# Kernel tuning notes

Hardware: AMD Instinct MI355X
Metric: run time of the kernel (lower is better)

## Reference

```python
import jax, jax.numpy as jnp
import numpy as np

NUM_HEADS = 8
KEY_DIM = 16
D_HEAD = 64  # attn_ratio(4) * key_dim


def setup_inputs() -> dict:
    key = jax.random.key(0)
    ks = jax.random.split(key, 13)
    f = jnp.float32
    x = jax.random.normal(ks[0], (2, 256, 56, 56), dtype=f)
    wq = jax.random.normal(ks[1], (128, 256), dtype=f) * 0.05
    sq = jax.random.uniform(ks[2], (128,), dtype=f)
    bq = jax.random.normal(ks[3], (128,), dtype=f) * 0.05
    wk = jax.random.normal(ks[4], (128, 256), dtype=f) * 0.05
    sk = jax.random.uniform(ks[5], (128,), dtype=f)
    bk = jax.random.normal(ks[6], (128,), dtype=f) * 0.05
    wv = jax.random.normal(ks[7], (512, 256), dtype=f) * 0.05
    sv = jax.random.uniform(ks[8], (512,), dtype=f)
    bv = jax.random.normal(ks[9], (512,), dtype=f) * 0.05
    wp = jax.random.normal(ks[10], (256, 512), dtype=f) * 0.05
    sp = jax.random.uniform(ks[11], (256,), dtype=f)
    bp = jax.random.normal(ks[12], (256,), dtype=f) * 0.05
    return dict(x=x, wq=wq, sq=sq, bq=bq, wk=wk, sk=sk, bk=bk,
                wv=wv, sv=sv, bv=bv, wp=wp, sp=sp, bp=bp)


def _conv1x1_bn(x, w, s, b):
    # 1x1 conv (no bias) + folded BatchNorm (eval): per-channel affine
    y = jnp.einsum('oc,bchw->bohw', w, x)
    return y * s[None, :, None, None] + b[None, :, None, None]


def reference(x, wq, sq, bq, wk, sk, bk, wv, sv, bv, wp, sp, bp):
    b, c, h, w = x.shape
    n = h * w
    q = _conv1x1_bn(x, wq, sq, bq).reshape(b, NUM_HEADS, KEY_DIM, n)
    k = _conv1x1_bn(x, wk, sk, bk).reshape(b, NUM_HEADS, KEY_DIM, n)
    v = _conv1x1_bn(x, wv, sv, bv).reshape(b, NUM_HEADS, D_HEAD, n)
    # scores: q^T k, NO 1/sqrt(key_dim) scaling (faithful to source)
    attn = jax.nn.softmax(jnp.einsum('bhdn,bhdm->bhnm', q, k), axis=-1)
    # out = attn @ v^T -> (b,h,n,d), then back to (b, dh, H, W)
    o = jnp.einsum('bhnm,bhdm->bhdn', attn, v).reshape(b, NUM_HEADS * D_HEAD, h, w)
    return _conv1x1_bn(o, wp, sp, bp)
```

## Files before the change

### kernel.cpp

```cpp
#include <hip/hip_runtime.h>


typedef short  s16x8 __attribute__((ext_vector_type(8)));
typedef float  f32x4 __attribute__((ext_vector_type(4)));
typedef unsigned short u16;
typedef unsigned short u16x4 __attribute__((ext_vector_type(4)));

__device__ __forceinline__ u16 f2bf(float f) {
    unsigned u = __builtin_bit_cast(unsigned, f);
    u += 0x7FFF + ((u >> 16) & 1);
    return (u16)(u >> 16);
}
__device__ __forceinline__ u16 f2bf_h(float f) {
    unsigned u = __builtin_bit_cast(unsigned, f);
    return (u16)((u + 0x8000) >> 16);
}
__device__ __forceinline__ f32x4 mfma32(s16x8 a, s16x8 b, f32x4 c) {
    return __builtin_amdgcn_mfma_f32_16x16x32_bf16(a, b, c, 0, 0, 0);
}

__global__ __launch_bounds__(256) void xtw_kernel(
    const float* __restrict__ x, u16* __restrict__ xpk,
    const float* __restrict__ wq, const float* __restrict__ sq,
    const float* __restrict__ wk, const float* __restrict__ sk,
    const float* __restrict__ wv, const float* __restrict__ sv,
    const float* __restrict__ wp, const float* __restrict__ sp,
    u16* __restrict__ wqpk, u16* __restrict__ wkpk,
    u16* __restrict__ wvpk, u16* __restrict__ wppk)
{
    const int t = threadIdx.x;
    if (blockIdx.z == 2) {
        int ch = (blockIdx.y * 49 + blockIdx.x) * 256 + t;
        const float *W, *S; u16* dst; int nkc;
        if (ch < 4096)        { W = wq; S = sq; dst = wqpk; nkc = 8; }
        else if (ch < 8192)   { W = wk; S = sk; dst = wkpk; nkc = 8;  ch -= 4096; }
        else if (ch < 24576)  { W = wv; S = sv; dst = wvpk; nkc = 8;  ch -= 8192; }
        else if (ch < 40960)  { W = wp; S = sp; dst = wppk; nkc = 16; ch -= 24576; }
        else return;
        const int lane = ch & 63, kc = (ch >> 6) % nkc, rt = (ch >> 6) / nkc;
        const int l15 = lane & 15, q = lane >> 4;
        const int row = rt * 16 + l15, C = nkc * 32;
        const float sc = S[row];
        const float* src = &W[row * C + kc * 32 + q * 8];
        s16x8 o;
        #pragma unroll
        for (int j = 0; j < 8; j++) o[j] = (short)f2bf(src[j] * sc);
        *(s16x8*)&dst[ch * 8] = o;
        return;
    }
    const int b = blockIdx.z, c0 = blockIdx.y * 64, n0 = blockIdx.x * 64;
    __shared__ float lds[64][65];
    const int nl = t & 63, cl = t >> 6;
    #pragma unroll
    for (int i = 0; i < 16; i++) {
        const int c = cl + i * 4;
        lds[c][nl] = x[(b * 256 + c0 + c) * 3136 + n0 + nl];
    }
    __syncthreads();
    #pragma unroll
    for (int rep = 0; rep < 2; rep++) {
        const int idx = rep * 256 + t;
        const int t16l = idx >> 7, kc8l = (idx >> 6) & 1, lane = idx & 63;
        const int l15 = lane & 15, q = lane >> 4;
        s16x8 o;
        #pragma unroll
        for (int j = 0; j < 8; j++)
            o[j] = (short)f2bf(lds[kc8l * 32 + q * 8 + j][t16l * 16 + l15]);
        const int tg = (n0 >> 4) + t16l, kg = (c0 >> 5) + kc8l;
        *(s16x8*)&xpk[(((b * 196 + tg) * 8 + kg) * 64 + lane) * 8] = o;
    }
}

__global__ __launch_bounds__(256, 4) void qkv_kernel(
    const u16* __restrict__ xpk,
    const u16* __restrict__ wqpk, const u16* __restrict__ wkpk, const u16* __restrict__ wvpk,
    const float* __restrict__ bq, const float* __restrict__ bk, const float* __restrict__ bv,
    u16* __restrict__ qws, u16* __restrict__ kws, u16* __restrict__ vpk)
{
    const int b = blockIdx.z, rt = blockIdx.y, n0 = blockIdx.x * 64;
    const int t = threadIdx.x, wave = t >> 6, lane = t & 63;
    const int l15 = lane & 15, quad = lane >> 4;
    const f32x4 z = {0.f, 0.f, 0.f, 0.f};

    if (rt < 4) {
        const u16* wb      = (rt < 2) ? wqpk : wkpk;
        const float* bias  = (rt < 2) ? bq : bk;
        u16* dst           = (rt < 2) ? qws : kws;
        const float qs     = (rt < 2) ? 1.44269504088896f : 1.0f;
        const int och0 = (rt & 1) * 64;
        const int m0   = n0 + wave * 16;
        const int m_t  = blockIdx.x * 4 + wave;
        s16x8 a8[8];
        #pragma unroll
        for (int kc8 = 0; kc8 < 8; kc8++)
            a8[kc8] = *(const s16x8*)&xpk[(((b * 196 + m_t) * 8 + kc8) * 64 + lane) * 8];
        f32x4 acc[4] = {z, z, z, z};
        #pragma unroll
        for (int kc8 = 0; kc8 < 8; kc8++) {
            #pragma unroll
            for (int f = 0; f < 4; f++) {
                s16x8 bf = *(const s16x8*)&wb[((((rt & 1) * 4 + f) * 8 + kc8) * 64 + lane) * 8];
                acc[f] = mfma32(a8[kc8], bf, acc[f]);
            }
        }
        #pragma unroll
        for (int f = 0; f < 4; f++) {
            const int och = och0 + f * 16 + l15;
            const float bi = bias[och];
            const int h = och >> 4;
            #pragma unroll
            for (int r = 0; r < 4; r++) {
                const int tok = m0 + quad * 4 + r;
                dst[((b * 8 + h) * 3136 + tok) * 16 + l15] = f2bf((acc[f][r] + bi) * qs);
            }
        }
    } else {
        const int h    = rt - 4;
        const int och0 = h * 64 + wave * 16;
        s16x8 a8[8];
        #pragma unroll
        for (int kc8 = 0; kc8 < 8; kc8++)
            a8[kc8] = *(const s16x8*)&wvpk[(((h * 4 + wave) * 8 + kc8) * 64 + lane) * 8];
        f32x4 acc[4] = {z, z, z, z};
        #pragma unroll
        for (int kc8 = 0; kc8 < 8; kc8++) {
            #pragma unroll
            for (int f = 0; f < 4; f++) {
                s16x8 bf = *(const s16x8*)&xpk[(((b * 196 + blockIdx.x * 4 + f) * 8 + kc8) * 64 + lane) * 8];
                acc[f] = mfma32(a8[kc8], bf, acc[f]);
            }
        }
        u16* vdst = &vpk[(((b * 8 + h) * 49 + blockIdx.x) * 8) * 512];
        #pragma unroll
        for (int r = 0; r < 4; r++) {
            const float bi = bv[och0 + quad * 4 + r];
            const int lane_r8 = ((l15 >> 2) * 16 + quad * 4 + r) * 8;
            #pragma unroll
            for (int f = 0; f < 4; f++) {
                const int idx = ((f >> 1) * 4 + wave) * 512 + lane_r8 + (f & 1) * 4 + (l15 & 3);
                vdst[idx] = f2bf(acc[f][r] + bi);
            }
        }
    }
}

__global__ __launch_bounds__(64) void attn_kernel(
    const u16* __restrict__ qws, const u16* __restrict__ kws,
    const u16* __restrict__ vpk, u16* __restrict__ opk)
{
    const int bh   = blockIdx.x;
    const int nb   = blockIdx.y * 32;
    const int lane = threadIdx.x;
    const int l15  = lane & 15, quad = lane >> 4;

    s16x8 aq[2];
    #pragma unroll
    for (int u = 0; u < 2; u++) {
        aq[u] = (s16x8){0, 0, 0, 0, 0, 0, 0, 0};
        if (quad < 2)
            aq[u] = *(const s16x8*)&qws[(bh * 3136 + nb + u * 16 + l15) * 16 + quad * 8];
    }
    s16x8 ones;
    #pragma unroll
    for (int i = 0; i < 8; i++) ones[i] = (short)0x3F80;

    const u16* krow = &kws[(bh * 3136 + l15) * 16 + (quad & 1) * 8];
    const u16* vb   = &vpk[bh * 49 * 4096 + lane * 8];

    f32x4 acc[2][4], acc5[2];
    #pragma unroll
    for (int u = 0; u < 2; u++) {
        #pragma unroll
        for (int dt = 0; dt < 4; dt++) acc[u][dt] = (f32x4){0.f, 0.f, 0.f, 0.f};
        acc5[u] = (f32x4){0.f, 0.f, 0.f, 0.f};
    }
    const f32x4 z = {0.f, 0.f, 0.f, 0.f};

    s16x8 kfA[4], vfA[8], kfB[4], vfB[8];
    auto loadK = [&](s16x8* kf, int c) {
        #pragma unroll
        for (int ii = 0; ii < 4; ii++)
            kf[ii] = *(const s16x8*)&krow[(c * 64 + ii * 16) * 16];
    };
    auto loadV = [&](s16x8* vf, int c) {
        #pragma unroll
        for (int i = 0; i < 8; i++)
            vf[i] = *(const s16x8*)&vb[(c * 8 + i) * 512];
    };
    auto compute = [&](const s16x8* kf, const s16x8* vf) {
        #pragma unroll
        for (int u = 0; u < 2; u++) {
            f32x4 s[4];
            #pragma unroll
            for (int ii = 0; ii < 4; ii++) s[ii] = mfma32(kf[ii], aq[u], z);
            s16x8 pf[2];
            #pragma unroll
            for (int c32 = 0; c32 < 2; c32++) {
                #pragma unroll
                for (int r = 0; r < 4; r++) {
                    pf[c32][r]     = (short)f2bf_h(__builtin_amdgcn_exp2f(s[2 * c32][r]));
                    pf[c32][4 + r] = (short)f2bf_h(__builtin_amdgcn_exp2f(s[2 * c32 + 1][r]));
                }
            }
            #pragma unroll
            for (int c32 = 0; c32 < 2; c32++) {
                #pragma unroll
                for (int dt = 0; dt < 4; dt++)
                    acc[u][dt] = mfma32(vf[c32 * 4 + dt], pf[c32], acc[u][dt]);
                acc5[u] = mfma32(ones, pf[c32], acc5[u]);
            }
        }
    };

    loadK(kfA, 0); loadV(vfA, 0);
    #pragma unroll 1
    for (int c = 0; c < 49; c += 2) {
        if (c + 1 < 49) { loadK(kfB, c + 1); loadV(vfB, c + 1); }
        compute(kfA, vfA);
        if (c + 2 < 49) { loadK(kfA, c + 2); loadV(vfA, c + 2); }
        if (c + 1 < 49) compute(kfB, vfB);
    }

    const int bq_ = bh >> 3, h = bh & 7;
    #pragma unroll
    for (int u = 0; u < 2; u++) {
        const float inv = 1.0f / acc5[u][0];
        const int tt = blockIdx.y * 2 + u;
        u16* ob = &opk[((bq_ * 196 + tt) * 16) * 512];
        #pragma unroll
        for (int dt = 0; dt < 4; dt++) {
            u16x4 o4;
            #pragma unroll
            for (int r = 0; r < 4; r++) o4[r] = f2bf(acc[u][dt][r] * inv);
            *(u16x4*)&ob[(h * 2 + (dt >> 1)) * 512 +
                         (((dt & 1) * 2 + (quad >> 1)) * 16 + l15) * 8 +
                         (quad & 1) * 4] = o4;
        }
    }
}

__global__ __launch_bounds__(256, 4) void proj_kernel(
    const u16* __restrict__ opk, const u16* __restrict__ wppk,
    const float* __restrict__ bp, float* __restrict__ out)
{
    const int b = blockIdx.z, n0 = blockIdx.x * 32;
    const int och0 = blockIdx.y * 64 + (threadIdx.x >> 6) * 16;
    const int lane = threadIdx.x & 63;
    const int l15 = lane & 15, quad = lane >> 4;
    const f32x4 z = {0.f, 0.f, 0.f, 0.f};

    const int och_t = blockIdx.y * 4 + (threadIdx.x >> 6);
    s16x8 a8[16];
    #pragma unroll
    for (int kc = 0; kc < 16; kc++)
        a8[kc] = *(const s16x8*)&wppk[((och_t * 16 + kc) * 64 + lane) * 8];
    f32x4 acc[2] = {z, z};
    #pragma unroll
    for (int kc = 0; kc < 16; kc++) {
        #pragma unroll
        for (int f = 0; f < 2; f++) {
            s16x8 bf = *(const s16x8*)&opk[(((b * 196 + blockIdx.x * 2 + f) * 16 + kc) * 64 + lane) * 8];
            acc[f] = mfma32(a8[kc], bf, acc[f]);
        }
    }
    #pragma unroll
    for (int r = 0; r < 4; r++) {
        const int och = och0 + quad * 4 + r;
        const float bi = bp[och];
        #pragma unroll
        for (int f = 0; f < 2; f++)
            out[(b * 256 + och) * 3136 + n0 + f * 16 + l15] = acc[f][r] + bi;
    }
}

extern "C" void kernel_launch(void* const* d_in, const int* in_sizes, int n_in,
                              void* d_out, int out_size, void* d_ws, size_t ws_size,
                              hipStream_t stream) {
    const float* x  = (const float*)d_in[0];
    const float* wq = (const float*)d_in[1];
    const float* sq = (const float*)d_in[2];
    const float* bq = (const float*)d_in[3];
    const float* wk = (const float*)d_in[4];
    const float* sk = (const float*)d_in[5];
    const float* bk = (const float*)d_in[6];
    const float* wv = (const float*)d_in[7];
    const float* sv = (const float*)d_in[8];
    const float* bv = (const float*)d_in[9];
    const float* wp = (const float*)d_in[10];
    const float* sp = (const float*)d_in[11];
    const float* bp = (const float*)d_in[12];
    float* out = (float*)d_out;

    u16* qws  = (u16*)d_ws;
    u16* kws  = qws + 802816;
    u16* vpk  = kws + 802816;
    u16* R    = vpk + 3211264;
    u16* xpk  = R;
    u16* opk  = R;
    u16* wqpk = R + 3211264;
    u16* wkpk = wqpk + 32768;
    u16* wvpk = wkpk + 32768;
    u16* wppk = wvpk + 131072;

    xtw_kernel<<<dim3(49, 4, 3), 256, 0, stream>>>(x, xpk, wq, sq, wk, sk,
                                                   wv, sv, wp, sp,
                                                   wqpk, wkpk, wvpk, wppk);
    qkv_kernel<<<dim3(49, 12, 2), 256, 0, stream>>>(xpk, wqpk, wkpk, wvpk,
                                                    bq, bk, bv, qws, kws, vpk);
    attn_kernel<<<dim3(16, 98), 64, 0, stream>>>(qws, kws, vpk, opk);
    proj_kernel<<<dim3(98, 4, 2), 256, 0, stream>>>(opk, wppk, bp, out);
}
```

Measured before the change: 152.2 us.

## Halve attention query tile per wave, use packed bf16 convert and setprio around MFMAs

The attention kernel now handles 16 query rows per 64-thread block instead of 32, doubling the grid to 16x196 blocks to raise occupancy and parallelism. In exchange, K and V tiles are reloaded twice as often for the same queries. The manual bf16 rounding of exp results is replaced by the packed v_cvt_pk_bf16_f32 instruction, cutting VALU work. s_setprio is raised around the PV MFMA block to favor matrix issue among co-resident waves.

```diff
diff --git a/kernel.cpp b/kernel.cpp
--- a/kernel.cpp
+++ b/kernel.cpp
@@ -3,6 +3,7 @@
 
 typedef short  s16x8 __attribute__((ext_vector_type(8)));
 typedef float  f32x4 __attribute__((ext_vector_type(4)));
+typedef int    i32x4 __attribute__((ext_vector_type(4)));
 typedef unsigned short u16;
 typedef unsigned short u16x4 __attribute__((ext_vector_type(4)));
 
@@ -11,12 +12,13 @@
     u += 0x7FFF + ((u >> 16) & 1);
     return (u16)(u >> 16);
 }
-__device__ __forceinline__ u16 f2bf_h(float f) {
-    unsigned u = __builtin_bit_cast(unsigned, f);
-    return (u16)((u + 0x8000) >> 16);
-}
 __device__ __forceinline__ f32x4 mfma32(s16x8 a, s16x8 b, f32x4 c) {
     return __builtin_amdgcn_mfma_f32_16x16x32_bf16(a, b, c, 0, 0, 0);
+}
+__device__ __forceinline__ int cvtpk(float lo, float hi) {
+    int r;
+    asm("v_cvt_pk_bf16_f32 %0, %1, %2" : "=v"(r) : "v"(lo), "v"(hi));
+    return r;
 }
 
 __global__ __launch_bounds__(256) void xtw_kernel(
@@ -149,17 +151,13 @@
     const u16* __restrict__ vpk, u16* __restrict__ opk)
 {
     const int bh   = blockIdx.x;
-    const int nb   = blockIdx.y * 32;
+    const int nb   = blockIdx.y * 16;
     const int lane = threadIdx.x;
     const int l15  = lane & 15, quad = lane >> 4;
 
-    s16x8 aq[2];
-    #pragma unroll
-    for (int u = 0; u < 2; u++) {
-        aq[u] = (s16x8){0, 0, 0, 0, 0, 0, 0, 0};
-        if (quad < 2)
-            aq[u] = *(const s16x8*)&qws[(bh * 3136 + nb + u * 16 + l15) * 16 + quad * 8];
-    }
+    s16x8 aq = {0, 0, 0, 0, 0, 0, 0, 0};
+    if (quad < 2)
+        aq = *(const s16x8*)&qws[(bh * 3136 + nb + l15) * 16 + quad * 8];
     s16x8 ones;
     #pragma unroll
     for (int i = 0; i < 8; i++) ones[i] = (short)0x3F80;
@@ -167,13 +165,10 @@
     const u16* krow = &kws[(bh * 3136 + l15) * 16 + (quad & 1) * 8];
     const u16* vb   = &vpk[bh * 49 * 4096 + lane * 8];
 
-    f32x4 acc[2][4], acc5[2];
-    #pragma unroll
-    for (int u = 0; u < 2; u++) {
-        #pragma unroll
-        for (int dt = 0; dt < 4; dt++) acc[u][dt] = (f32x4){0.f, 0.f, 0.f, 0.f};
-        acc5[u] = (f32x4){0.f, 0.f, 0.f, 0.f};
-    }
+    f32x4 acc[4], acc5;
+    #pragma unroll
+    for (int dt = 0; dt < 4; dt++) acc[dt] = (f32x4){0.f, 0.f, 0.f, 0.f};
+    acc5 = (f32x4){0.f, 0.f, 0.f, 0.f};
     const f32x4 z = {0.f, 0.f, 0.f, 0.f};
 
     s16x8 kfA[4], vfA[8], kfB[4], vfB[8];
@@ -188,28 +183,34 @@
             vf[i] = *(const s16x8*)&vb[(c * 8 + i) * 512];
     };
     auto compute = [&](const s16x8* kf, const s16x8* vf) {
-        #pragma unroll
-        for (int u = 0; u < 2; u++) {
-            f32x4 s[4];
-            #pragma unroll
-            for (int ii = 0; ii < 4; ii++) s[ii] = mfma32(kf[ii], aq[u], z);
-            s16x8 pf[2];
-            #pragma unroll
-            for (int c32 = 0; c32 < 2; c32++) {
-                #pragma unroll
-                for (int r = 0; r < 4; r++) {
-                    pf[c32][r]     = (short)f2bf_h(__builtin_amdgcn_exp2f(s[2 * c32][r]));
-                    pf[c32][4 + r] = (short)f2bf_h(__builtin_amdgcn_exp2f(s[2 * c32 + 1][r]));
-                }
-            }
-            #pragma unroll
-            for (int c32 = 0; c32 < 2; c32++) {
-                #pragma unroll
-                for (int dt = 0; dt < 4; dt++)
-                    acc[u][dt] = mfma32(vf[c32 * 4 + dt], pf[c32], acc[u][dt]);
-                acc5[u] = mfma32(ones, pf[c32], acc5[u]);
-            }
-        }
+        f32x4 s[4];
+        #pragma unroll
+        for (int ii = 0; ii < 4; ii++) s[ii] = mfma32(kf[ii], aq, z);
+        float e[4][4];
+        #pragma unroll
+        for (int ii = 0; ii < 4; ii++)
+            #pragma unroll
+            for (int r = 0; r < 4; r++)
+                e[ii][r] = __builtin_amdgcn_exp2f(s[ii][r]);
+        s16x8 pf[2];
+        #pragma unroll
+        for (int c32 = 0; c32 < 2; c32++) {
+            i32x4 pk;
+            pk[0] = cvtpk(e[2 * c32][0],     e[2 * c32][1]);
+            pk[1] = cvtpk(e[2 * c32][2],     e[2 * c32][3]);
+            pk[2] = cvtpk(e[2 * c32 + 1][0], e[2 * c32 + 1][1]);
+            pk[3] = cvtpk(e[2 * c32 + 1][2], e[2 * c32 + 1][3]);
+            pf[c32] = __builtin_bit_cast(s16x8, pk);
+        }
+        __builtin_amdgcn_s_setprio(1);
+        #pragma unroll
+        for (int c32 = 0; c32 < 2; c32++) {
+            #pragma unroll
+            for (int dt = 0; dt < 4; dt++)
+                acc[dt] = mfma32(vf[c32 * 4 + dt], pf[c32], acc[dt]);
+            acc5 = mfma32(ones, pf[c32], acc5);
+        }
+        __builtin_amdgcn_s_setprio(0);
     };
 
     loadK(kfA, 0); loadV(vfA, 0);
@@ -222,20 +223,16 @@
     }
 
     const int bq_ = bh >> 3, h = bh & 7;
-    #pragma unroll
-    for (int u = 0; u < 2; u++) {
-        const float inv = 1.0f / acc5[u][0];
-        const int tt = blockIdx.y * 2 + u;
-        u16* ob = &opk[((bq_ * 196 + tt) * 16) * 512];
-        #pragma unroll
-        for (int dt = 0; dt < 4; dt++) {
-            u16x4 o4;
-            #pragma unroll
-            for (int r = 0; r < 4; r++) o4[r] = f2bf(acc[u][dt][r] * inv);
-            *(u16x4*)&ob[(h * 2 + (dt >> 1)) * 512 +
-                         (((dt & 1) * 2 + (quad >> 1)) * 16 + l15) * 8 +
-                         (quad & 1) * 4] = o4;
-        }
+    const float inv = 1.0f / acc5[0];
+    u16* ob = &opk[((bq_ * 196 + blockIdx.y) * 16) * 512];
+    #pragma unroll
+    for (int dt = 0; dt < 4; dt++) {
+        u16x4 o4;
+        #pragma unroll
+        for (int r = 0; r < 4; r++) o4[r] = f2bf(acc[dt][r] * inv);
+        *(u16x4*)&ob[(h * 2 + (dt >> 1)) * 512 +
+                     (((dt & 1) * 2 + (quad >> 1)) * 16 + l15) * 8 +
+                     (quad & 1) * 4] = o4;
     }
 }
 
@@ -307,6 +304,6 @@
                                                    wqpk, wkpk, wvpk, wppk);
     qkv_kernel<<<dim3(49, 12, 2), 256, 0, stream>>>(xpk, wqpk, wkpk, wvpk,
                                                     bq, bk, bv, qws, kws, vpk);
-    attn_kernel<<<dim3(16, 98), 64, 0, stream>>>(qws, kws, vpk, opk);
+    attn_kernel<<<dim3(16, 196), 64, 0, stream>>>(qws, kws, vpk, opk);
     proj_kernel<<<dim3(98, 4, 2), 256, 0, stream>>>(opk, wppk, bp, out);
 }
```

Result: slower. 169.9 us (+11.6%).
